# Kernel optimization log

Measured on AMD Instinct MI355X. Metric: run time of the kernel, lower is better.

The kernel has to match this reference:

```python
import jax, jax.numpy as jnp
import numpy as np

B, S, H, E, V = 64, 512, 1024, 512, 32000
D = 2  # bidirectional encoder -> memory dim = D*H


def setup_inputs() -> dict:
    key = jax.random.key(0)
    ks = jax.random.split(key, 16)
    sc = lambda n: 1.0 / np.sqrt(n)
    return {
        "word": jax.random.randint(ks[0], (B,), 1, V),
        "hidden": jax.random.normal(ks[1], (B, H), jnp.float32),
        "encoder_outputs": jax.random.normal(ks[2], (B, S, D * H), jnp.float32),
        "output_distribution": jax.random.uniform(ks[3], (B, V), jnp.float32),
        "encoder_attention": jax.random.uniform(ks[4], (B, S), jnp.float32),
        # embedding (padding_idx=0 row zeroed)
        "emb": jax.random.normal(ks[5], (V, E), jnp.float32).at[0].set(0.0) * 0.02,
        # Bah_Attn params
        "lin1_w": jax.random.normal(ks[6], (H, H), jnp.float32) * sc(H),
        "lin1_b": jnp.zeros((H,), jnp.float32),
        "lin2_w": jax.random.normal(ks[7], (H, D * H), jnp.float32) * sc(D * H),
        "lin2_b": jnp.zeros((H,), jnp.float32),
        "v_w": jax.random.normal(ks[8], (1, H), jnp.float32) * sc(H),
        "v_b": jnp.zeros((1,), jnp.float32),
        # GRUCell params: input = context(2H) + word_vec(E) = 2560
        "W_ih": jax.random.normal(ks[9], (3 * H, D * H + E), jnp.float32) * sc(H),
        "b_ih": jnp.zeros((3 * H,), jnp.float32),
        "W_hh": jax.random.normal(ks[10], (3 * H, H), jnp.float32) * sc(H),
        "b_hh": jnp.zeros((3 * H,), jnp.float32),
        # output projection
        "out_w": jax.random.normal(ks[11], (V, H), jnp.float32) * sc(H),
        "out_b": jnp.zeros((V,), jnp.float32),
    }


def reference(word, hidden, encoder_outputs, output_distribution, encoder_attention,
              emb, lin1_w, lin1_b, lin2_w, lin2_b, v_w, v_b,
              W_ih, b_ih, W_hh, b_hh, out_w, out_b):
    # word embedding lookup (feed_word_emb='word')
    word_vec = emb[word]                                   # [B, E]
    h_x = hidden @ lin1_w.T + lin1_b                       # [B, H]
    h_m = jnp.einsum('bsm,hm->bsh', encoder_outputs, lin2_w) + lin2_b  # [B, S, H]
    e = jnp.tanh(h_x[:, None, :] + h_m) @ v_w[0] + v_b[0]  # [B, S]
    score = jax.nn.softmax(e, axis=-1)                     # [B, S]
    context = jnp.einsum('bs,bsm->bm', score, encoder_outputs)  # [B, 2H]
    # GRUCell step on cat([context, word_vec])
    x = jnp.concatenate([context, word_vec], axis=1)       # [B, 2H+E]
    gi = x @ W_ih.T + b_ih                                 # [B, 3H]
    gh = hidden @ W_hh.T + b_hh                            # [B, 3H]
    i_r, i_z, i_n = jnp.split(gi, 3, axis=1)
    h_r, h_z, h_n = jnp.split(gh, 3, axis=1)
    r = jax.nn.sigmoid(i_r + h_r)
    z = jax.nn.sigmoid(i_z + h_z)
    n = jnp.tanh(i_n + r * h_n)
    new_hidden = (1.0 - z) * n + z * hidden                # [B, H]
    pred_word = new_hidden @ out_w.T + out_b               # [B, V]
    return (pred_word, new_hidden, score)
```

## Files before the change

### kernel.cpp

```cpp
#include <hip/hip_runtime.h>
#include <hip/hip_bf16.h>
#include <stdint.h>

typedef __attribute__((ext_vector_type(4))) float f32x4;
typedef __attribute__((ext_vector_type(8))) short short8;

#define B_   64
#define S_   512
#define H_   1024
#define E_   512
#define V_   32000
#define M_   2048
#define BS_  32768
#define XIN_ 2560
#define G3_  3072

__device__ __forceinline__ unsigned short f2bf(float f) {
  union { float f; unsigned u; } x; x.f = f;
  unsigned r = x.u + 0x7fffu + ((x.u >> 16) & 1u);
  return (unsigned short)(r >> 16);
}

__device__ __forceinline__ float bf2f(unsigned short u) {
  union { unsigned u; float f; } x; x.u = (unsigned)u << 16; return x.f;
}

__device__ __forceinline__ void async16(const void* g, void* l) {
  __builtin_amdgcn_global_load_lds((const __attribute__((address_space(1))) unsigned*)g,
                                   (__attribute__((address_space(3))) unsigned*)l,
                                   16, 0, 0);
}

__global__ __launch_bounds__(256) void k_convhx(const float* __restrict__ enc,
                                                unsigned short* __restrict__ ebf,
                                                const float* __restrict__ lin2w,
                                                unsigned short* __restrict__ bw,
                                                const int* __restrict__ word,
                                                const float* __restrict__ emb,
                                                float* __restrict__ wv,
                                                const float* __restrict__ hidden,
                                                const float* __restrict__ w1,
                                                const float* __restrict__ b1,
                                                const float* __restrict__ b2,
                                                float* __restrict__ hx) {
  __shared__ float hs[64][36];
  __shared__ float Ws[64][36];
  const int t = threadIdx.x;
  if (blockIdx.x >= 4096) {
    const int hbase = (blockIdx.x - 4096) * 64;
    const int hb = t & 15, bb = t >> 4;
    const int srow = t >> 2, sc0 = (t & 3) * 8;
    float acc[4][4] = {};
    for (int kc = 0; kc < H_; kc += 32) {
      *(f32x4*)&hs[srow][sc0]     = *(const f32x4*)(hidden + (size_t)srow * H_ + kc + sc0);
      *(f32x4*)&hs[srow][sc0 + 4] = *(const f32x4*)(hidden + (size_t)srow * H_ + kc + sc0 + 4);
      *(f32x4*)&Ws[srow][sc0]     = *(const f32x4*)(w1 + (size_t)(hbase + srow) * H_ + kc + sc0);
      *(f32x4*)&Ws[srow][sc0 + 4] = *(const f32x4*)(w1 + (size_t)(hbase + srow) * H_ + kc + sc0 + 4);
      __syncthreads();
#pragma unroll
      for (int kk = 0; kk < 32; ++kk) {
        float a[4], w4[4];
#pragma unroll
        for (int i = 0; i < 4; ++i) a[i] = hs[bb * 4 + i][kk];
#pragma unroll
        for (int j = 0; j < 4; ++j) w4[j] = Ws[hb + 16 * j][kk];
#pragma unroll
        for (int i = 0; i < 4; ++i)
#pragma unroll
          for (int j = 0; j < 4; ++j) acc[i][j] += a[i] * w4[j];
      }
      __syncthreads();
    }
#pragma unroll
    for (int i = 0; i < 4; ++i)
#pragma unroll
      for (int j = 0; j < 4; ++j) {
        int h = hbase + hb + 16 * j;
        hx[(size_t)(bb * 4 + i) * H_ + h] = acc[i][j] + b1[h] + b2[h];
      }
    return;
  }
  const size_t NENC8 = (size_t)BS_ * M_ / 8;
  const size_t NW8   = (size_t)H_ * M_ / 8;
  const size_t NWV4  = (size_t)B_ * E_ / 4;
  const size_t total = NENC8 + NW8 + NWV4;
  for (size_t idx = (size_t)blockIdx.x * 256 + t; idx < total;
       idx += (size_t)4096 * 256) {
    if (idx < NENC8) {
      f32x4 a = *(const f32x4*)(enc + idx * 8);
      f32x4 b = *(const f32x4*)(enc + idx * 8 + 4);
      short8 o = { (short)f2bf(a.x), (short)f2bf(a.y), (short)f2bf(a.z), (short)f2bf(a.w),
                   (short)f2bf(b.x), (short)f2bf(b.y), (short)f2bf(b.z), (short)f2bf(b.w) };
      *(short8*)(ebf + idx * 8) = o;
    } else if (idx < NENC8 + NW8) {
      size_t i = idx - NENC8;
      f32x4 a = *(const f32x4*)(lin2w + i * 8);
      f32x4 b = *(const f32x4*)(lin2w + i * 8 + 4);
      short8 o = { (short)f2bf(a.x), (short)f2bf(a.y), (short)f2bf(a.z), (short)f2bf(a.w),
                   (short)f2bf(b.x), (short)f2bf(b.y), (short)f2bf(b.z), (short)f2bf(b.w) };
      *(short8*)(bw + i * 8) = o;
    } else {
      size_t i = idx - NENC8 - NW8;
      int i0 = (int)i * 4;
      int b = i0 >> 9, c = i0 & 511;
      f32x4 v = *(const f32x4*)(emb + (size_t)word[b] * E_ + c);
      *(f32x4*)(wv + i0) = v;
    }
  }
}

__global__ __launch_bounds__(512, 2) void k_attn3(const unsigned short* __restrict__ encbf,
                                                  const unsigned short* __restrict__ bw,
                                                  const float* __restrict__ hx,
                                                  const float* __restrict__ vw,
                                                  float* __restrict__ epart) {
  extern __shared__ char smem[];
  const int t = threadIdx.x;
  const int w8 = t >> 6, l = t & 63;
  const int wm = w8 >> 1, wn = w8 & 1;
  const int l15 = l & 15, l4 = l >> 4;
  const int bid = blockIdx.x;
  const int xcd = bid & 7, idx = bid >> 3;
  const int bm = xcd * 16 + (idx >> 2);
  const int bn = idx & 3;
  const int b = bm >> 1;

  f32x4 acc[4][8] = {};

  const unsigned short* Ag = encbf + (size_t)(bm * 256) * M_;
  const unsigned short* Bg = bw + (size_t)(bn * 256) * M_;

  const int lr = l >> 2, lc = l & 3;
  const int sw = (lr >> 1) & 3;
  const unsigned short* aSrc0 = Ag + (size_t)(w8 * 32 + lr) * M_ + (lc ^ sw) * 8;
  const unsigned short* aSrc1 = aSrc0 + (size_t)16 * M_;
  const unsigned short* bSrc0 = Bg + (size_t)(w8 * 32 + lr) * M_ + (lc ^ sw) * 8;
  const unsigned short* bSrc1 = bSrc0 + (size_t)16 * M_;
  const int slotoff = (l4 ^ ((l15 >> 1) & 3)) * 16;

#define STAGE(buf, kt) do { const int k0 = (kt) * 32;                       \
    char* base_ = smem + (buf) * 32768;                                     \
    async16(aSrc0 + k0, base_ + w8 * 2048 + l * 16);                        \
    async16(aSrc1 + k0, base_ + w8 * 2048 + 1024 + l * 16);                 \
    async16(bSrc0 + k0, base_ + 16384 + w8 * 2048 + l * 16);                \
    async16(bSrc1 + k0, base_ + 16384 + w8 * 2048 + 1024 + l * 16); } while (0)

  STAGE(0, 0);
  STAGE(1, 1);
  asm volatile("s_waitcnt vmcnt(4)" ::: "memory");
  __builtin_amdgcn_s_barrier();

  int cur = 0;
  for (int kt = 0; kt < 64; ++kt) {
    int nx2 = cur + 2; if (nx2 >= 3) nx2 -= 3;
    if (kt < 62) STAGE(nx2, kt + 2);
    const char* aBase = smem + cur * 32768;
    const char* bBase = aBase + 16384;
    short8 af[4], bf[8];
#pragma unroll
    for (int m = 0; m < 4; ++m)
      af[m] = *(const short8*)(aBase + (wm * 64 + m * 16 + l15) * 64 + slotoff);
#pragma unroll
    for (int n = 0; n < 8; ++n)
      bf[n] = *(const short8*)(bBase + (wn * 128 + n * 16 + l15) * 64 + slotoff);
    __builtin_amdgcn_s_setprio(1);
#pragma unroll
    for (int m = 0; m < 4; ++m)
#pragma unroll
      for (int n = 0; n < 8; ++n)
        acc[m][n] = __builtin_amdgcn_mfma_f32_16x16x32_bf16(af[m], bf[n], acc[m][n], 0, 0, 0);
    __builtin_amdgcn_s_setprio(0);
    if (kt < 62) {
      asm volatile("s_waitcnt vmcnt(4)" ::: "memory");
    } else {
      asm volatile("s_waitcnt vmcnt(0)" ::: "memory");
    }
    __builtin_amdgcn_s_barrier();
    cur = cur + 1; if (cur >= 3) cur = 0;
  }
#undef STAGE

  const int rbase = bm * 256 + wm * 64;
  const int colbase = bn * 256 + wn * 128;
  const int part = bn * 2 + wn;
#pragma unroll
  for (int m = 0; m < 4; ++m) {
#pragma unroll
    for (int j = 0; j < 4; ++j) {
      int rg = rbase + m * 16 + l4 * 4 + j;
      float sum = 0.f;
#pragma unroll
      for (int n = 0; n < 8; ++n) {
        int h = colbase + n * 16 + l15;
        sum += vw[h] * tanhf(hx[b * H_ + h] + acc[m][n][j]);
      }
      sum += __shfl_xor(sum, 1);
      sum += __shfl_xor(sum, 2);
      sum += __shfl_xor(sum, 4);
      sum += __shfl_xor(sum, 8);
      if (l15 == 0) epart[(size_t)part * BS_ + rg] = sum;
    }
  }
}

__global__ __launch_bounds__(512, 4) void k_attn2(const unsigned short* __restrict__ encbf,
                                                  const unsigned short* __restrict__ bw,
                                                  const float* __restrict__ hx,
                                                  const float* __restrict__ vw,
                                                  float* __restrict__ epart) {
  extern __shared__ char smem[];
  const int t = threadIdx.x;
  const int w8 = t >> 6, l = t & 63;
  const int wm = w8 >> 1, wn = w8 & 1;
  const int l15 = l & 15, l4 = l >> 4;
  const int bid = blockIdx.x;
  const int xcd = bid & 7, idx = bid >> 3;
  const int bm = xcd * 16 + (idx >> 3);
  const int bn = idx & 7;
  const int b = bm >> 1;

  f32x4 acc[4][4] = {};

  const unsigned short* Ag = encbf + (size_t)(bm * 256) * M_;
  const unsigned short* Bg = bw + (size_t)(bn * 128) * M_;

  const int lr = l >> 2, lc = l & 3;
  const int sw = (lr >> 1) & 3;
  const unsigned short* aSrc0 = Ag + (size_t)(w8 * 32 + lr) * M_ + (lc ^ sw) * 8;
  const unsigned short* aSrc1 = aSrc0 + (size_t)16 * M_;
  const unsigned short* bSrc  = Bg + (size_t)(w8 * 16 + lr) * M_ + (lc ^ sw) * 8;
  const int slotoff = (l4 ^ ((l15 >> 1) & 3)) * 16;

#define STAGE(buf, kt) do { const int k0 = (kt) * 32;                       \
    char* base_ = smem + (buf) * 24576;                                     \
    async16(aSrc0 + k0, base_ + w8 * 2048 + l * 16);                        \
    async16(aSrc1 + k0, base_ + w8 * 2048 + 1024 + l * 16);                 \
    async16(bSrc  + k0, base_ + 16384 + w8 * 1024 + l * 16); } while (0)

  STAGE(0, 0);
  STAGE(1, 1);
  asm volatile("s_waitcnt vmcnt(3)" ::: "memory");
  __builtin_amdgcn_s_barrier();

  int cur = 0;
  for (int kt = 0; kt < 64; ++kt) {
    int nx2 = cur + 2; if (nx2 >= 3) nx2 -= 3;
    if (kt < 62) STAGE(nx2, kt + 2);
    const char* aBase = smem + cur * 24576;
    const char* bBase = aBase + 16384;
    short8 af[4], bf[4];
#pragma unroll
    for (int m = 0; m < 4; ++m)
      af[m] = *(const short8*)(aBase + (wm * 64 + m * 16 + l15) * 64 + slotoff);
#pragma unroll
    for (int n = 0; n < 4; ++n)
      bf[n] = *(const short8*)(bBase + (wn * 64 + n * 16 + l15) * 64 + slotoff);
    __builtin_amdgcn_s_setprio(1);
#pragma unroll
    for (int m = 0; m < 4; ++m)
#pragma unroll
      for (int n = 0; n < 4; ++n)
        acc[m][n] = __builtin_amdgcn_mfma_f32_16x16x32_bf16(af[m], bf[n], acc[m][n], 0, 0, 0);
    __builtin_amdgcn_s_setprio(0);
    if (kt < 62) {
      asm volatile("s_waitcnt vmcnt(3)" ::: "memory");
    } else {
      asm volatile("s_waitcnt vmcnt(0)" ::: "memory");
    }
    __builtin_amdgcn_s_barrier();
    cur = cur + 1; if (cur >= 3) cur = 0;
  }
#undef STAGE

  const int rbase = bm * 256 + wm * 64;
  const int colbase = bn * 128 + wn * 64;
  const int part = bn * 2 + wn;
#pragma unroll
  for (int m = 0; m < 4; ++m) {
#pragma unroll
    for (int j = 0; j < 4; ++j) {
      int rg = rbase + m * 16 + l4 * 4 + j;
      float sum = 0.f;
#pragma unroll
      for (int n = 0; n < 4; ++n) {
        int h = colbase + n * 16 + l15;
        sum += vw[h] * tanhf(hx[b * H_ + h] + acc[m][n][j]);
      }
      sum += __shfl_xor(sum, 1);
      sum += __shfl_xor(sum, 2);
      sum += __shfl_xor(sum, 4);
      sum += __shfl_xor(sum, 8);
      if (l15 == 0) epart[(size_t)part * BS_ + rg] = sum;
    }
  }
}

__global__ __launch_bounds__(256) void k_attn(const float* __restrict__ enc,
                                              const unsigned short* __restrict__ bw,
                                              const float* __restrict__ hx,
                                              const float* __restrict__ vw,
                                              float* __restrict__ epart) {
  __shared__ unsigned short As[128 * 32];
  __shared__ unsigned short Bs[128 * 32];
  const int bid = blockIdx.x;
  const int bm = bid & 255, bn = bid >> 8;
  const int t = threadIdx.x;
  const int l = t & 63, w = t >> 6;
  const int wr = w >> 1, wc = w & 1;
  const int l15 = l & 15, l4 = l >> 4;

  f32x4 acc[4][4] = {};

  const float* Ag = enc + (size_t)(bm * 128) * M_;
  const unsigned short* Bg = bw + (size_t)(bn * 128) * M_;

  const int ar = t >> 3;
  const int ac = (t & 7) * 4;
  const int br = t >> 2;
  const int bc = (t & 3) * 8;

  for (int kt = 0; kt < 64; ++kt) {
    const int k0 = kt * 32;
    async16(Bg + (size_t)br * M_ + k0 + bc, (char*)Bs + (size_t)t * 16);
    async16(Bg + (size_t)(br + 64) * M_ + k0 + bc, (char*)Bs + 4096 + (size_t)t * 16);
#pragma unroll
    for (int j = 0; j < 4; ++j) {
      f32x4 v = *(const f32x4*)(Ag + (size_t)(ar + j * 32) * M_ + k0 + ac);
      ushort4 o = { f2bf(v.x), f2bf(v.y), f2bf(v.z), f2bf(v.w) };
      *(ushort4*)(As + (ar + j * 32) * 32 + ac) = o;
    }
    __syncthreads();
    short8 af[4], bf[4];
#pragma unroll
    for (int m = 0; m < 4; ++m)
      af[m] = *(const short8*)(As + (wr * 64 + m * 16 + l15) * 32 + l4 * 8);
#pragma unroll
    for (int n = 0; n < 4; ++n)
      bf[n] = *(const short8*)(Bs + (wc * 64 + n * 16 + l15) * 32 + l4 * 8);
#pragma unroll
    for (int m = 0; m < 4; ++m)
#pragma unroll
      for (int n = 0; n < 4; ++n)
        acc[m][n] = __builtin_amdgcn_mfma_f32_16x16x32_bf16(af[m], bf[n], acc[m][n], 0, 0, 0);
    __syncthreads();
  }

  const int colbase = bn * 128 + wc * 64;
#pragma unroll
  for (int m = 0; m < 4; ++m) {
#pragma unroll
    for (int j = 0; j < 4; ++j) {
      int rloc = wr * 64 + m * 16 + l4 * 4 + j;
      int rg = bm * 128 + rloc;
      int b = rg >> 9;
      float sum = 0.f;
#pragma unroll
      for (int n = 0; n < 4; ++n) {
        int h = colbase + n * 16 + l15;
        sum += vw[h] * tanhf(hx[b * H_ + h] + acc[m][n][j]);
      }
      sum += __shfl_xor(sum, 1);
      sum += __shfl_xor(sum, 2);
      sum += __shfl_xor(sum, 4);
      sum += __shfl_xor(sum, 8);
      if (l15 == 0) epart[(size_t)(bn * 2 + wc) * BS_ + rg] = sum;
    }
  }
}

__global__ __launch_bounds__(256) void k_softmax(const float* __restrict__ epart,
                                                 float* __restrict__ score,
                                                 int npart) {
  int b = blockIdx.x, t = threadIdx.x;
  float v0 = 0.f, v1 = 0.f;
  for (int p = 0; p < npart; ++p) {
    v0 += epart[(size_t)p * BS_ + b * S_ + t];
    v1 += epart[(size_t)p * BS_ + b * S_ + 256 + t];
  }
  int w = t >> 6, l = t & 63;
  float m = fmaxf(v0, v1);
#pragma unroll
  for (int off = 32; off; off >>= 1) m = fmaxf(m, __shfl_xor(m, off));
  __shared__ float sm[4];
  __shared__ float ssum[4];
  if (l == 0) sm[w] = m;
  __syncthreads();
  float M = fmaxf(fmaxf(sm[0], sm[1]), fmaxf(sm[2], sm[3]));
  float p0 = expf(v0 - M), p1 = expf(v1 - M);
  float s = p0 + p1;
#pragma unroll
  for (int off = 32; off; off >>= 1) s += __shfl_xor(s, off);
  if (l == 0) ssum[w] = s;
  __syncthreads();
  float inv = 1.f / (ssum[0] + ssum[1] + ssum[2] + ssum[3]);
  score[b * S_ + t] = p0 * inv;
  score[b * S_ + 256 + t] = p1 * inv;
}

__global__ __launch_bounds__(256) void k_ctxb(const unsigned short* __restrict__ encbf,
                                              const float* __restrict__ score,
                                              float* __restrict__ cpart) {
  int blk = blockIdx.x;
  int b = blk >> 3, sc = blk & 7;
  int t = threadIdx.x;
  int m = t * 8;
  f32x4 acc0 = {0.f, 0.f, 0.f, 0.f}, acc1 = {0.f, 0.f, 0.f, 0.f};
  const unsigned short* ep = encbf + (size_t)(b * S_ + sc * 64) * M_ + m;
  const float* sp = score + b * S_ + sc * 64;
#pragma unroll 4
  for (int s8 = 0; s8 < 64; ++s8) {
    float sv = sp[s8];
    short8 v = *(const short8*)(ep + (size_t)s8 * M_);
    acc0.x += bf2f((unsigned short)v[0]) * sv;
    acc0.y += bf2f((unsigned short)v[1]) * sv;
    acc0.z += bf2f((unsigned short)v[2]) * sv;
    acc0.w += bf2f((unsigned short)v[3]) * sv;
    acc1.x += bf2f((unsigned short)v[4]) * sv;
    acc1.y += bf2f((unsigned short)v[5]) * sv;
    acc1.z += bf2f((unsigned short)v[6]) * sv;
    acc1.w += bf2f((unsigned short)v[7]) * sv;
  }
  float* dst = cpart + (size_t)sc * (B_ * M_) + b * M_ + m;
  *(f32x4*)dst = acc0;
  *(f32x4*)(dst + 4) = acc1;
}

__global__ __launch_bounds__(256) void k_ctx(const float* __restrict__ enc,
                                             const float* __restrict__ score,
                                             float* __restrict__ cpart) {
  int blk = blockIdx.x;
  int b = blk >> 4, mc = (blk >> 3) & 1, sc = blk & 7;
  int t = threadIdx.x;
  int m = mc * 1024 + t * 4;
  f32x4 acc = {0.f, 0.f, 0.f, 0.f};
  const float* ep = enc + (size_t)b * S_ * M_ + m;
  const float* sp = score + b * S_ + sc * 64;
#pragma unroll 4
  for (int s8 = 0; s8 < 64; ++s8) {
    float sv = sp[s8];
    f32x4 v = *(const f32x4*)(ep + (size_t)(sc * 64 + s8) * M_);
    acc += v * sv;
  }
  *(f32x4*)(cpart + (size_t)sc * (B_ * M_) + b * M_ + m) = acc;
}

__global__ void k_ctxred(const float* __restrict__ cpart, float* __restrict__ ctx) {
  int i0 = (blockIdx.x * 256 + threadIdx.x) * 4;
  f32x4 a = {0.f, 0.f, 0.f, 0.f};
#pragma unroll
  for (int p = 0; p < 8; ++p) a += *(const f32x4*)(cpart + (size_t)p * (B_ * M_) + i0);
  *(f32x4*)(ctx + i0) = a;
}

__global__ __launch_bounds__(256) void k_grugemm(const float* __restrict__ ctx,
                                                 const float* __restrict__ wv,
                                                 const float* __restrict__ hidden,
                                                 const float* __restrict__ Wih,
                                                 const float* __restrict__ bih,
                                                 const float* __restrict__ Whh,
                                                 const float* __restrict__ bhh,
                                                 float* __restrict__ gi0,
                                                 float* __restrict__ gi1,
                                                 float* __restrict__ gh0,
                                                 float* __restrict__ gh1) {
  __shared__ float xs[64][36];
  __shared__ float Ws[64][36];
  const int t = threadIdx.x;
  const int blk = blockIdx.x;
  const bool ghh = blk >= 96;
  const int sub = ghh ? blk - 96 : blk;
  const int colt = sub % 48, half = sub / 48;
  const int gbase = colt * 64;
  const int K = ghh ? H_ : XIN_;
  const int klo = ghh ? (half ? 512 : 0) : (half ? 1280 : 0);
  const int khi = ghh ? (half ? 1024 : 512) : (half ? 2560 : 1280);
  const float* Wp = ghh ? Whh : Wih;
  const int vb = t & 15, bb = t >> 4;
  const int srow = t >> 2, sc0 = (t & 3) * 8;
  float acc[4][4] = {};
  for (int kc = klo; kc < khi; kc += 32) {
    f32x4 xa, xb;
    if (ghh) {
      xa = *(const f32x4*)(hidden + (size_t)srow * H_ + kc + sc0);
      xb = *(const f32x4*)(hidden + (size_t)srow * H_ + kc + sc0 + 4);
    } else if (kc + sc0 < M_) {
      xa = *(const f32x4*)(ctx + (size_t)srow * M_ + kc + sc0);
      xb = *(const f32x4*)(ctx + (size_t)srow * M_ + kc + sc0 + 4);
    } else {
      xa = *(const f32x4*)(wv + (size_t)srow * E_ + kc + sc0 - M_);
      xb = *(const f32x4*)(wv + (size_t)srow * E_ + kc + sc0 - M_ + 4);
    }
    *(f32x4*)&xs[srow][sc0] = xa;
    *(f32x4*)&xs[srow][sc0 + 4] = xb;
    *(f32x4*)&Ws[srow][sc0]     = *(const f32x4*)(Wp + (size_t)(gbase + srow) * K + kc + sc0);
    *(f32x4*)&Ws[srow][sc0 + 4] = *(const f32x4*)(Wp + (size_t)(gbase + srow) * K + kc + sc0 + 4);
    __syncthreads();
#pragma unroll
    for (int kk = 0; kk < 32; ++kk) {
      float a[4], w4[4];
#pragma unroll
      for (int i = 0; i < 4; ++i) a[i] = xs[bb * 4 + i][kk];
#pragma unroll
      for (int j = 0; j < 4; ++j) w4[j] = Ws[vb + 16 * j][kk];
#pragma unroll
      for (int i = 0; i < 4; ++i)
#pragma unroll
        for (int j = 0; j < 4; ++j) acc[i][j] += a[i] * w4[j];
    }
    __syncthreads();
  }
  float* dst = ghh ? (half ? gh1 : gh0) : (half ? gi1 : gi0);
  const float* bias = ghh ? bhh : bih;
#pragma unroll
  for (int i = 0; i < 4; ++i)
#pragma unroll
    for (int j = 0; j < 4; ++j) {
      int g = gbase + vb + 16 * j;
      float v = acc[i][j] + (half ? 0.f : bias[g]);
      dst[(size_t)(bb * 4 + i) * G3_ + g] = v;
    }
}

__global__ void k_gate(const float* __restrict__ gi0, const float* __restrict__ gi1,
                       const float* __restrict__ gh0, const float* __restrict__ gh1,
                       const float* __restrict__ hidden, float* __restrict__ newh,
                       unsigned short* __restrict__ newhbf) {
  int o = blockIdx.x * 256 + threadIdx.x;
  int b = o >> 10, h = o & 1023;
  size_t base = (size_t)b * G3_;
  float ir = gi0[base + h] + gi1[base + h];
  float iz = gi0[base + 1024 + h] + gi1[base + 1024 + h];
  float in = gi0[base + 2048 + h] + gi1[base + 2048 + h];
  float hr = gh0[base + h] + gh1[base + h];
  float hz = gh0[base + 1024 + h] + gh1[base + 1024 + h];
  float hn = gh0[base + 2048 + h] + gh1[base + 2048 + h];
  float r = 1.f / (1.f + expf(-(ir + hr)));
  float z = 1.f / (1.f + expf(-(iz + hz)));
  float n = tanhf(in + r * hn);
  float nh = (1.f - z) * n + z * hidden[o];
  newh[o] = nh;
  newhbf[o] = f2bf(nh);
}

__global__ __launch_bounds__(256) void k_outproj_mfma(const unsigned short* __restrict__ newhbf,
                                                      const float* __restrict__ ow,
                                                      const float* __restrict__ ob,
                                                      float* __restrict__ pred) {
  __shared__ unsigned short As[2048];
  __shared__ unsigned short Bs[4096];
  const int t = threadIdx.x;
  const int w = t >> 6, l = t & 63;
  const int l15 = l & 15, l4 = l >> 4;
  const int vbase = blockIdx.x * 128;

  const unsigned short* aSrc = newhbf + (size_t)(t & 63) * H_ + (t >> 6) * 8;
  const int br = t >> 1, bh = t & 1;
  const float* bSrc = ow + (size_t)(vbase + br) * H_ + bh * 16;

  f32x4 acc[4][2] = {};

  for (int kc = 0; kc < H_; kc += 32) {
    async16(aSrc + kc, (char*)As + (size_t)t * 16);
    f32x4 v0 = *(const f32x4*)(bSrc + kc);
    f32x4 v1 = *(const f32x4*)(bSrc + kc + 4);
    f32x4 v2 = *(const f32x4*)(bSrc + kc + 8);
    f32x4 v3 = *(const f32x4*)(bSrc + kc + 12);
    ushort4 p0 = { f2bf(v0.x), f2bf(v0.y), f2bf(v0.z), f2bf(v0.w) };
    ushort4 p1 = { f2bf(v1.x), f2bf(v1.y), f2bf(v1.z), f2bf(v1.w) };
    ushort4 p2 = { f2bf(v2.x), f2bf(v2.y), f2bf(v2.z), f2bf(v2.w) };
    ushort4 p3 = { f2bf(v3.x), f2bf(v3.y), f2bf(v3.z), f2bf(v3.w) };
    const int kg0 = bh * 2;
    *(ushort4*)(Bs + kg0 * 1024 + br * 8)       = p0;
    *(ushort4*)(Bs + kg0 * 1024 + br * 8 + 4)   = p1;
    *(ushort4*)(Bs + (kg0 + 1) * 1024 + br * 8)     = p2;
    *(ushort4*)(Bs + (kg0 + 1) * 1024 + br * 8 + 4) = p3;
    __syncthreads();
    short8 af[4], bf[2];
#pragma unroll
    for (int rf = 0; rf < 4; ++rf)
      af[rf] = *(const short8*)(As + l4 * 512 + (rf * 16 + l15) * 8);
#pragma unroll
    for (int cf = 0; cf < 2; ++cf)
      bf[cf] = *(const short8*)(Bs + l4 * 1024 + (w * 32 + cf * 16 + l15) * 8);
#pragma unroll
    for (int rf = 0; rf < 4; ++rf)
#pragma unroll
      for (int cf = 0; cf < 2; ++cf)
        acc[rf][cf] = __builtin_amdgcn_mfma_f32_16x16x32_bf16(af[rf], bf[cf], acc[rf][cf], 0, 0, 0);
    __syncthreads();
  }

#pragma unroll
  for (int cf = 0; cf < 2; ++cf) {
    int col = vbase + w * 32 + cf * 16 + l15;
    float bias = ob[col];
#pragma unroll
    for (int rf = 0; rf < 4; ++rf)
#pragma unroll
      for (int j = 0; j < 4; ++j) {
        int row = rf * 16 + l4 * 4 + j;
        pred[(size_t)row * V_ + col] = acc[rf][cf][j] + bias;
      }
  }
}

extern "C" void kernel_launch(void* const* d_in, const int* in_sizes, int n_in,
                              void* d_out, int out_size, void* d_ws, size_t ws_size,
                              hipStream_t stream) {
  const int*   word   = (const int*)d_in[0];
  const float* hidden = (const float*)d_in[1];
  const float* enc    = (const float*)d_in[2];
  const float* emb    = (const float*)d_in[5];
  const float* lin1w  = (const float*)d_in[6];
  const float* lin1b  = (const float*)d_in[7];
  const float* lin2w  = (const float*)d_in[8];
  const float* lin2b  = (const float*)d_in[9];
  const float* vw     = (const float*)d_in[10];
  const float* Wih    = (const float*)d_in[12];
  const float* bih    = (const float*)d_in[13];
  const float* Whh    = (const float*)d_in[14];
  const float* bhh    = (const float*)d_in[15];
  const float* ow     = (const float*)d_in[16];
  const float* ob     = (const float*)d_in[17];

  float* out   = (float*)d_out;
  float* pred  = out;
  float* newh  = out + 2048000;
  float* score = out + 2113536;

  const size_t ENCBF = 134217728;
  const bool fast = ws_size >= ENCBF + 13107200;
  char* ws = (char*)d_ws;
  unsigned short* encbf = (unsigned short*)ws;
  size_t base = fast ? ENCBF : 0;
  unsigned short* bw = (unsigned short*)(ws + base);
  float* hx    = (float*)(ws + base + 4194304);
  float* wvbuf = (float*)(ws + base + 4456448);
  float* epart = (float*)(ws + base + 4587520);
  float* cpart = (float*)(ws + base + 6684672);
  float* ctx   = (float*)(ws + base + 10878976);
  float* gi0   = (float*)(ws + base + 11403264);
  float* gh0   = (float*)(ws + base + 12189696);
  unsigned short* nhbf = (unsigned short*)(ws + base + 12976128);
  float* gi1   = epart;
  float* gh1   = epart + 196608;

  bool use3 = false, use2 = false;
  if (fast) {
    use3 = (hipFuncSetAttribute((const void*)k_attn3,
        hipFuncAttributeMaxDynamicSharedMemorySize, 98304) == hipSuccess);
    if (!use3)
      use2 = (hipFuncSetAttribute((const void*)k_attn2,
          hipFuncAttributeMaxDynamicSharedMemorySize, 73728) == hipSuccess);
  }

  if (fast) {
    k_convhx<<<4112, 256, 0, stream>>>(enc, encbf, lin2w, bw, word, emb, wvbuf,
                                       hidden, lin1w, lin1b, lin2b, hx);
    int npart;
    if (use3) {
      k_attn3<<<512, 512, 98304, stream>>>(encbf, bw, hx, vw, epart);
      npart = 8;
    } else if (use2) {
      k_attn2<<<1024, 512, 73728, stream>>>(encbf, bw, hx, vw, epart);
      npart = 16;
    } else {
      k_attn<<<2048, 256, 0, stream>>>((const float*)d_in[2], bw, hx, vw, epart);
      npart = 16;
    }
    k_softmax<<<64, 256, 0, stream>>>(epart, score, npart);
    k_ctxb<<<512, 256, 0, stream>>>(encbf, score, cpart);
  } else {
    k_convhx<<<4112, 256, 0, stream>>>(enc, encbf, lin2w, bw, word, emb, wvbuf,
                                       hidden, lin1w, lin1b, lin2b, hx);
    k_attn<<<2048, 256, 0, stream>>>(enc, bw, hx, vw, epart);
    k_softmax<<<64, 256, 0, stream>>>(epart, score, 16);
    k_ctx<<<1024, 256, 0, stream>>>(enc, score, cpart);
  }
  k_ctxred<<<128, 256, 0, stream>>>(cpart, ctx);
  k_grugemm<<<192, 256, 0, stream>>>(ctx, wvbuf, hidden, Wih, bih, Whh, bhh, gi0, gi1, gh0, gh1);
  k_gate<<<256, 256, 0, stream>>>(gi0, gi1, gh0, gh1, hidden, newh, nhbf);
  k_outproj_mfma<<<250, 256, 0, stream>>>(nhbf, ow, ob, pred);
}
```

Measured before the change: 452.1 us.

## Split encoder bf16 conversion into own kernel and coalesce out_w loads

Splits the fused conversion kernel in two. One kernel streams encoder_outputs to bf16 with nontemporal loads and four independent 16-byte loads per thread instead of a grid-stride loop. A second kernel handles the lin2 weight conversion, embedding gather and the hidden@lin1 GEMM. The output-projection kernel now has 8 threads cover one 128-byte row segment when loading out_w, which improves coalescing, and each thread handles 4 rows. This adds one kernel launch, and the nontemporal hint may cost L2 reuse if later kernels reread the fp32 encoder buffer.

```diff
diff --git a/kernel.cpp b/kernel.cpp
--- a/kernel.cpp
+++ b/kernel.cpp
@@ -15,6 +15,16 @@
 #define XIN_ 2560
 #define G3_  3072
 
+#if defined(__has_builtin)
+#if __has_builtin(__builtin_nontemporal_load)
+#define NT_LOAD(p) __builtin_nontemporal_load(p)
+#else
+#define NT_LOAD(p) (*(p))
+#endif
+#else
+#define NT_LOAD(p) (*(p))
+#endif
+
 __device__ __forceinline__ unsigned short f2bf(float f) {
   union { float f; unsigned u; } x; x.f = f;
   unsigned r = x.u + 0x7fffu + ((x.u >> 16) & 1u);
@@ -31,82 +41,80 @@
                                    16, 0, 0);
 }
 
-__global__ __launch_bounds__(256) void k_convhx(const float* __restrict__ enc,
-                                                unsigned short* __restrict__ ebf,
-                                                const float* __restrict__ lin2w,
-                                                unsigned short* __restrict__ bw,
-                                                const int* __restrict__ word,
-                                                const float* __restrict__ emb,
-                                                float* __restrict__ wv,
-                                                const float* __restrict__ hidden,
-                                                const float* __restrict__ w1,
-                                                const float* __restrict__ b1,
-                                                const float* __restrict__ b2,
-                                                float* __restrict__ hx) {
+__global__ __launch_bounds__(256) void k_enc2bf(const float* __restrict__ enc,
+                                                unsigned short* __restrict__ ebf) {
+  const size_t i0 = (size_t)blockIdx.x * 1024 + threadIdx.x;
+  f32x4 v[4];
+#pragma unroll
+  for (int p = 0; p < 4; ++p)
+    v[p] = NT_LOAD((const f32x4*)enc + i0 + p * 256);
+#pragma unroll
+  for (int p = 0; p < 4; ++p) {
+    ushort4 o = { f2bf(v[p].x), f2bf(v[p].y), f2bf(v[p].z), f2bf(v[p].w) };
+    *(ushort4*)(ebf + (i0 + p * 256) * 4) = o;
+  }
+}
+
+__global__ __launch_bounds__(256) void k_prep2(const float* __restrict__ lin2w,
+                                               unsigned short* __restrict__ bw,
+                                               const int* __restrict__ word,
+                                               const float* __restrict__ emb,
+                                               float* __restrict__ wv,
+                                               const float* __restrict__ hidden,
+                                               const float* __restrict__ w1,
+                                               const float* __restrict__ b1,
+                                               const float* __restrict__ b2,
+                                               float* __restrict__ hx) {
   __shared__ float hs[64][36];
   __shared__ float Ws[64][36];
   const int t = threadIdx.x;
-  if (blockIdx.x >= 4096) {
-    const int hbase = (blockIdx.x - 4096) * 64;
-    const int hb = t & 15, bb = t >> 4;
-    const int srow = t >> 2, sc0 = (t & 3) * 8;
-    float acc[4][4] = {};
-    for (int kc = 0; kc < H_; kc += 32) {
-      *(f32x4*)&hs[srow][sc0]     = *(const f32x4*)(hidden + (size_t)srow * H_ + kc + sc0);
-      *(f32x4*)&hs[srow][sc0 + 4] = *(const f32x4*)(hidden + (size_t)srow * H_ + kc + sc0 + 4);
-      *(f32x4*)&Ws[srow][sc0]     = *(const f32x4*)(w1 + (size_t)(hbase + srow) * H_ + kc + sc0);
-      *(f32x4*)&Ws[srow][sc0 + 4] = *(const f32x4*)(w1 + (size_t)(hbase + srow) * H_ + kc + sc0 + 4);
-      __syncthreads();
-#pragma unroll
-      for (int kk = 0; kk < 32; ++kk) {
-        float a[4], w4[4];
-#pragma unroll
-        for (int i = 0; i < 4; ++i) a[i] = hs[bb * 4 + i][kk];
-#pragma unroll
-        for (int j = 0; j < 4; ++j) w4[j] = Ws[hb + 16 * j][kk];
-#pragma unroll
-        for (int i = 0; i < 4; ++i)
-#pragma unroll
-          for (int j = 0; j < 4; ++j) acc[i][j] += a[i] * w4[j];
-      }
-      __syncthreads();
-    }
-#pragma unroll
-    for (int i = 0; i < 4; ++i)
-#pragma unroll
-      for (int j = 0; j < 4; ++j) {
-        int h = hbase + hb + 16 * j;
-        hx[(size_t)(bb * 4 + i) * H_ + h] = acc[i][j] + b1[h] + b2[h];
-      }
+  const int blk = blockIdx.x;
+  if (blk < 2048) {
+    size_t i = (size_t)blk * 256 + t;
+    f32x4 v = *((const f32x4*)lin2w + i);
+    ushort4 o = { f2bf(v.x), f2bf(v.y), f2bf(v.z), f2bf(v.w) };
+    *(ushort4*)(bw + i * 4) = o;
     return;
   }
-  const size_t NENC8 = (size_t)BS_ * M_ / 8;
-  const size_t NW8   = (size_t)H_ * M_ / 8;
-  const size_t NWV4  = (size_t)B_ * E_ / 4;
-  const size_t total = NENC8 + NW8 + NWV4;
-  for (size_t idx = (size_t)blockIdx.x * 256 + t; idx < total;
-       idx += (size_t)4096 * 256) {
-    if (idx < NENC8) {
-      f32x4 a = *(const f32x4*)(enc + idx * 8);
-      f32x4 b = *(const f32x4*)(enc + idx * 8 + 4);
-      short8 o = { (short)f2bf(a.x), (short)f2bf(a.y), (short)f2bf(a.z), (short)f2bf(a.w),
-                   (short)f2bf(b.x), (short)f2bf(b.y), (short)f2bf(b.z), (short)f2bf(b.w) };
-      *(short8*)(ebf + idx * 8) = o;
-    } else if (idx < NENC8 + NW8) {
-      size_t i = idx - NENC8;
-      f32x4 a = *(const f32x4*)(lin2w + i * 8);
-      f32x4 b = *(const f32x4*)(lin2w + i * 8 + 4);
-      short8 o = { (short)f2bf(a.x), (short)f2bf(a.y), (short)f2bf(a.z), (short)f2bf(a.w),
-                   (short)f2bf(b.x), (short)f2bf(b.y), (short)f2bf(b.z), (short)f2bf(b.w) };
-      *(short8*)(bw + i * 8) = o;
-    } else {
-      size_t i = idx - NENC8 - NW8;
-      int i0 = (int)i * 4;
-      int b = i0 >> 9, c = i0 & 511;
-      f32x4 v = *(const f32x4*)(emb + (size_t)word[b] * E_ + c);
-      *(f32x4*)(wv + i0) = v;
-    }
-  }
+  if (blk < 2080) {
+    int i = (blk - 2048) * 256 + t;
+    int i0 = i * 4;
+    int b = i0 >> 9, c = i0 & 511;
+    f32x4 v = *(const f32x4*)(emb + (size_t)word[b] * E_ + c);
+    *(f32x4*)(wv + i0) = v;
+    return;
+  }
+  const int hbase = (blk - 2080) * 64;
+  const int hb = t & 15, bb = t >> 4;
+  const int srow = t >> 2, sc0 = (t & 3) * 8;
+  float acc[4][4] = {};
+  for (int kc = 0; kc < H_; kc += 32) {
+    *(f32x4*)&hs[srow][sc0]     = *(const f32x4*)(hidden + (size_t)srow * H_ + kc + sc0);
+    *(f32x4*)&hs[srow][sc0 + 4] = *(const f32x4*)(hidden + (size_t)srow * H_ + kc + sc0 + 4);
+    *(f32x4*)&Ws[srow][sc0]     = *(const f32x4*)(w1 + (size_t)(hbase + srow) * H_ + kc + sc0);
+    *(f32x4*)&Ws[srow][sc0 + 4] = *(const f32x4*)(w1 + (size_t)(hbase + srow) * H_ + kc + sc0 + 4);
+    __syncthreads();
+#pragma unroll
+    for (int kk = 0; kk < 32; ++kk) {
+      float a[4], w4[4];
+#pragma unroll
+      for (int i = 0; i < 4; ++i) a[i] = hs[bb * 4 + i][kk];
+#pragma unroll
+      for (int j = 0; j < 4; ++j) w4[j] = Ws[hb + 16 * j][kk];
+#pragma unroll
+      for (int i = 0; i < 4; ++i)
+#pragma unroll
+        for (int j = 0; j < 4; ++j) acc[i][j] += a[i] * w4[j];
+    }
+    __syncthreads();
+  }
+#pragma unroll
+  for (int i = 0; i < 4; ++i)
+#pragma unroll
+    for (int j = 0; j < 4; ++j) {
+      int h = hbase + hb + 16 * j;
+      hx[(size_t)(bb * 4 + i) * H_ + h] = acc[i][j] + b1[h] + b2[h];
+    }
 }
 
 __global__ __launch_bounds__(512, 2) void k_attn3(const unsigned short* __restrict__ encbf,
@@ -554,26 +562,23 @@
   const int vbase = blockIdx.x * 128;
 
   const unsigned short* aSrc = newhbf + (size_t)(t & 63) * H_ + (t >> 6) * 8;
-  const int br = t >> 1, bh = t & 1;
-  const float* bSrc = ow + (size_t)(vbase + br) * H_ + bh * 16;
+  const int brow = t >> 3, bcol = (t & 7) * 4;
+  const float* bSrc = ow + (size_t)(vbase + brow) * H_ + bcol;
+  const int kg = (t & 7) >> 1, koff = (t & 1) * 4;
 
   f32x4 acc[4][2] = {};
 
   for (int kc = 0; kc < H_; kc += 32) {
     async16(aSrc + kc, (char*)As + (size_t)t * 16);
-    f32x4 v0 = *(const f32x4*)(bSrc + kc);
-    f32x4 v1 = *(const f32x4*)(bSrc + kc + 4);
-    f32x4 v2 = *(const f32x4*)(bSrc + kc + 8);
-    f32x4 v3 = *(const f32x4*)(bSrc + kc + 12);
-    ushort4 p0 = { f2bf(v0.x), f2bf(v0.y), f2bf(v0.z), f2bf(v0.w) };
-    ushort4 p1 = { f2bf(v1.x), f2bf(v1.y), f2bf(v1.z), f2bf(v1.w) };
-    ushort4 p2 = { f2bf(v2.x), f2bf(v2.y), f2bf(v2.z), f2bf(v2.w) };
-    ushort4 p3 = { f2bf(v3.x), f2bf(v3.y), f2bf(v3.z), f2bf(v3.w) };
-    const int kg0 = bh * 2;
-    *(ushort4*)(Bs + kg0 * 1024 + br * 8)       = p0;
-    *(ushort4*)(Bs + kg0 * 1024 + br * 8 + 4)   = p1;
-    *(ushort4*)(Bs + (kg0 + 1) * 1024 + br * 8)     = p2;
-    *(ushort4*)(Bs + (kg0 + 1) * 1024 + br * 8 + 4) = p3;
+    f32x4 vv[4];
+#pragma unroll
+    for (int p = 0; p < 4; ++p)
+      vv[p] = *(const f32x4*)(bSrc + kc + (size_t)p * 32 * H_);
+#pragma unroll
+    for (int p = 0; p < 4; ++p) {
+      ushort4 o = { f2bf(vv[p].x), f2bf(vv[p].y), f2bf(vv[p].z), f2bf(vv[p].w) };
+      *(ushort4*)(Bs + kg * 1024 + (brow + p * 32) * 8 + koff) = o;
+    }
     __syncthreads();
     short8 af[4], bf[2];
 #pragma unroll
@@ -654,9 +659,10 @@
           hipFuncAttributeMaxDynamicSharedMemorySize, 73728) == hipSuccess);
   }
 
+  k_prep2<<<2096, 256, 0, stream>>>(lin2w, bw, word, emb, wvbuf,
+                                    hidden, lin1w, lin1b, lin2b, hx);
   if (fast) {
-    k_convhx<<<4112, 256, 0, stream>>>(enc, encbf, lin2w, bw, word, emb, wvbuf,
-                                       hidden, lin1w, lin1b, lin2b, hx);
+    k_enc2bf<<<16384, 256, 0, stream>>>(enc, encbf);
     int npart;
     if (use3) {
       k_attn3<<<512, 512, 98304, stream>>>(encbf, bw, hx, vw, epart);
@@ -665,14 +671,12 @@
       k_attn2<<<1024, 512, 73728, stream>>>(encbf, bw, hx, vw, epart);
       npart = 16;
     } else {
-      k_attn<<<2048, 256, 0, stream>>>((const float*)d_in[2], bw, hx, vw, epart);
+      k_attn<<<2048, 256, 0, stream>>>(enc, bw, hx, vw, epart);
       npart = 16;
     }
     k_softmax<<<64, 256, 0, stream>>>(epart, score, npart);
     k_ctxb<<<512, 256, 0, stream>>>(encbf, score, cpart);
   } else {
-    k_convhx<<<4112, 256, 0, stream>>>(enc, encbf, lin2w, bw, word, emb, wvbuf,
-                                       hidden, lin1w, lin1b, lin2b, hx);
     k_attn<<<2048, 256, 0, stream>>>(enc, bw, hx, vw, epart);
     k_softmax<<<64, 256, 0, stream>>>(epart, score, 16);
     k_ctx<<<1024, 256, 0, stream>>>(enc, score, cpart);
```

Result: no change. 459.0 us (+1.5%).
